# Kernel tuning notes

Measured on AMD Instinct MI355X. Metric: run time of the kernel, lower is better.

Reference implementation:

```python
import jax, jax.numpy as jnp
import numpy as np

IMG_DIM = 512
BATCH = 32


def setup_inputs() -> dict:
    key = jax.random.key(0)
    k1, k2, k3, k4, k5 = jax.random.split(key, 5)
    N, D = BATCH, IMG_DIM
    return {
        "im1": jax.random.normal(k1, (N, 3, D, D), jnp.float32),
        "im2": jax.random.normal(k2, (N, 3, D, D), jnp.float32),
        "C": jax.random.normal(k3, (N, 2, D, D), jnp.float32),
        "M1": jax.random.uniform(k4, (N, 1, D, D), jnp.float32),
        "M2": jax.random.uniform(k5, (N, 1, D, D), jnp.float32),
    }


def _grid_q(D):
    # q[0] = row coord repeated, q[1] = col coord tiled -> [2, D*D]
    x = jnp.arange(D, dtype=jnp.float32)
    return jnp.stack([jnp.repeat(x, D), jnp.tile(x, D)], axis=0)


def _get_pixel(qi, nb_x, nb_y, imflat, D):
    # qi: [N,2,HW]; nb_x, nb_y: [N,HW] integer-valued floats; imflat: [N,3,HW]
    w = (1.0 - jnp.abs(qi[:, 0] - nb_x)) * (1.0 - jnp.abs(qi[:, 1] - nb_y))  # [N,HW]
    inds = (nb_y + D * nb_x).astype(jnp.int32)  # ind = y + D*x, detached from grads
    inds = jax.lax.stop_gradient(inds)
    px = jnp.take_along_axis(imflat, inds[:, None, :], axis=2)  # [N,3,HW]
    return w[:, None, :] * px


def _masked_rp(image, mask, qi_orig, D):
    N = image.shape[0]
    HW = D * D
    imflat = image.reshape(N, 3, HW)
    qi = jnp.clip(qi_orig, 0.001, D - 1.001)  # [N,2,HW]
    fx, fy = jnp.floor(qi[:, 0]), jnp.floor(qi[:, 1])
    cx, cy = jnp.ceil(qi[:, 0]), jnp.ceil(qi[:, 1])
    res = (_get_pixel(qi, fx, fy, imflat, D)
           + _get_pixel(qi, cx, fy, imflat, D)
           + _get_pixel(qi, fx, cy, imflat, D)
           + _get_pixel(qi, cx, cy, imflat, D))  # [N,3,HW]
    oob_loss = jnp.mean((qi_orig - qi) ** 2) / (D * D) * 0.01
    res_img = res.reshape(image.shape)
    return res_img * mask, oob_loss


def _forward(im1, im2, C, M1, M2):
    N = im1.shape[0]
    D = im1.shape[2]
    q = _grid_q(D)[None]  # [1,2,HW]
    Cflat = C.reshape(N, 2, D * D)
    a, la = _masked_rp(im1, M1, q + Cflat, D)
    b, lb = _masked_rp(im2, M2, q - Cflat, D)
    return a + b, la + lb


def reference(im1, im2, C, M1, M2):
    return _forward(im1, im2, C, M1, M2)
```

## Files before the change

kernel.cpp:

```cpp
#include <hip/hip_runtime.h>


constexpr int D    = 512;
constexpr int HW   = D * D;
constexpr int NB   = 32;
constexpr int NPIX = NB * HW;
constexpr float LOSS_SCALE = (float)(0.01 / (2.0 * (double)NPIX * (double)HW));

__device__ __forceinline__ float3 sample_img(const float* __restrict__ im,
                                             float q0o, float q1o, float& oob)
{
    const float hi = (float)(512.0 - 1.001);
    float q0 = fminf(fmaxf(q0o, 0.001f), hi);
    float q1 = fminf(fmaxf(q1o, 0.001f), hi);
    float d0 = q0o - q0, d1 = q1o - q1;
    oob += d0 * d0 + d1 * d1;

    float fx = floorf(q0), fy = floorf(q1);
    float cx = ceilf(q0),  cy = ceilf(q1);
    float wfx = 1.0f - (q0 - fx), wcx = 1.0f - (cx - q0);
    float wfy = 1.0f - (q1 - fy), wcy = 1.0f - (cy - q1);

    int ix0 = (int)fx, iy0 = (int)fy, ix1 = (int)cx, iy1 = (int)cy;
    int iff = iy0 + D * ix0;
    int icf = iy0 + D * ix1;
    int ifc = iy1 + D * ix0;
    int icc = iy1 + D * ix1;

    float wff = wfx * wfy, wcf = wcx * wfy, wfc = wfx * wcy, wcc = wcx * wcy;

    float3 r;
    r.x = wff * im[iff]          + wcf * im[icf]          + wfc * im[ifc]          + wcc * im[icc];
    r.y = wff * im[HW + iff]     + wcf * im[HW + icf]     + wfc * im[HW + ifc]     + wcc * im[HW + icc];
    r.z = wff * im[2 * HW + iff] + wcf * im[2 * HW + icf] + wfc * im[2 * HW + ifc] + wcc * im[2 * HW + icc];
    return r;
}

__global__ void __launch_bounds__(256)
vm_fwd(const float* __restrict__ im1, const float* __restrict__ im2,
       const float* __restrict__ C,   const float* __restrict__ M1,
       const float* __restrict__ M2,  float* __restrict__ out)
{
    float oob = 0.0f;
    int stride = gridDim.x * blockDim.x;
    for (int idx = blockIdx.x * blockDim.x + threadIdx.x; idx < NPIX; idx += stride) {
        int n  = idx >> 18;
        int hw = idx & (HW - 1);
        float qx = (float)(hw >> 9);
        float qy = (float)(hw & (D - 1));

        const float* Cn = C + (size_t)n * 2 * HW;
        float c0 = Cn[hw];
        float c1 = Cn[HW + hw];
        float m1 = M1[idx];
        float m2 = M2[idx];

        const float* p1 = im1 + (size_t)n * 3 * HW;
        const float* p2 = im2 + (size_t)n * 3 * HW;

        float3 a = sample_img(p1, qx + c0, qy + c1, oob);
        float3 b = sample_img(p2, qx - c0, qy - c1, oob);

        size_t obase = (size_t)n * 3 * HW + hw;
        out[obase]          = a.x * m1 + b.x * m2;
        out[obase + HW]     = a.y * m1 + b.y * m2;
        out[obase + 2 * HW] = a.z * m1 + b.z * m2;
    }

    #pragma unroll
    for (int off = 32; off > 0; off >>= 1)
        oob += __shfl_down(oob, off, 64);

    __shared__ float wave_sums[4];
    int lane = threadIdx.x & 63;
    int wave = threadIdx.x >> 6;
    if (lane == 0) wave_sums[wave] = oob;
    __syncthreads();
    if (threadIdx.x == 0) {
        float s = wave_sums[0] + wave_sums[1] + wave_sums[2] + wave_sums[3];
        atomicAdd(out + (size_t)3 * NPIX, s * LOSS_SCALE);
    }
}

extern "C" void kernel_launch(void* const* d_in, const int* in_sizes, int n_in,
                              void* d_out, int out_size, void* d_ws, size_t ws_size,
                              hipStream_t stream) {
    const float* im1 = (const float*)d_in[0];
    const float* im2 = (const float*)d_in[1];
    const float* C   = (const float*)d_in[2];
    const float* M1  = (const float*)d_in[3];
    const float* M2  = (const float*)d_in[4];
    float* out = (float*)d_out;

    hipMemsetAsync(out + (size_t)3 * NPIX, 0, sizeof(float), stream);

    vm_fwd<<<8192, 256, 0, stream>>>(im1, im2, C, M1, M2, out);
}
```

Before: 417.2 us.

## Process four pixels per thread with vector loads and paired-column gathers

Each thread now handles four consecutive pixels, using float4 nontemporal loads for the flow field and masks and float4 nontemporal stores for the output. The bilinear gather fetches adjacent y neighbours as one unaligned 2-float load per row, which cuts the gather instruction count in half. The grid-stride loop is replaced by an exact launch of NPIX/1024 blocks. The trade-offs are higher register pressure and unaligned paired loads that can read one element past a row, which stays in bounds because the sample is clamped below 510.999.

```diff
diff --git a/kernel.cpp b/kernel.cpp
--- a/kernel.cpp
+++ b/kernel.cpp
@@ -7,33 +7,48 @@
 constexpr int NPIX = NB * HW;
 constexpr float LOSS_SCALE = (float)(0.01 / (2.0 * (double)NPIX * (double)HW));
 
-__device__ __forceinline__ float3 sample_img(const float* __restrict__ im,
-                                             float q0o, float q1o, float& oob)
+typedef float f4  __attribute__((ext_vector_type(4)));
+typedef float f2a4 __attribute__((ext_vector_type(2), aligned(4)));
+
+__device__ __forceinline__ f2a4 ld2(const float* p) {
+    return *(const f2a4*)p;
+}
+
+__device__ __forceinline__ void sample_add(const float* __restrict__ im,
+                                           float q0o, float q1o, float m,
+                                           float& oob, float& ax, float& ay, float& az)
 {
-    const float hi = (float)(512.0 - 1.001);
+    const float hi = 510.999f;
     float q0 = fminf(fmaxf(q0o, 0.001f), hi);
     float q1 = fminf(fmaxf(q1o, 0.001f), hi);
     float d0 = q0o - q0, d1 = q1o - q1;
     oob += d0 * d0 + d1 * d1;
 
-    float fx = floorf(q0), fy = floorf(q1);
-    float cx = ceilf(q0),  cy = ceilf(q1);
+    float fx = floorf(q0), cx = ceilf(q0);
+    float fy = floorf(q1), cy = ceilf(q1);
     float wfx = 1.0f - (q0 - fx), wcx = 1.0f - (cx - q0);
     float wfy = 1.0f - (q1 - fy), wcy = 1.0f - (cy - q1);
 
-    int ix0 = (int)fx, iy0 = (int)fy, ix1 = (int)cx, iy1 = (int)cy;
-    int iff = iy0 + D * ix0;
-    int icf = iy0 + D * ix1;
-    int ifc = iy1 + D * ix0;
-    int icc = iy1 + D * ix1;
+    int ix0 = (int)fx, ix1 = (int)cx, iy0 = (int)fy;
+    bool ysame = ((int)cy == iy0);
 
-    float wff = wfx * wfy, wcf = wcx * wfy, wfc = wfx * wcy, wcc = wcx * wcy;
+    int off0 = (ix0 << 9) + iy0;
+    int off1 = (ix1 << 9) + iy0;
 
-    float3 r;
-    r.x = wff * im[iff]          + wcf * im[icf]          + wfc * im[ifc]          + wcc * im[icc];
-    r.y = wff * im[HW + iff]     + wcf * im[HW + icf]     + wfc * im[HW + ifc]     + wcc * im[HW + icc];
-    r.z = wff * im[2 * HW + iff] + wcf * im[2 * HW + icf] + wfc * im[2 * HW + ifc] + wcc * im[2 * HW + icc];
-    return r;
+    f2a4 r0x = ld2(im + off0);
+    f2a4 r1x = ld2(im + off1);
+    f2a4 r0y = ld2(im + HW + off0);
+    f2a4 r1y = ld2(im + HW + off1);
+    f2a4 r0z = ld2(im + 2 * HW + off0);
+    f2a4 r1z = ld2(im + 2 * HW + off1);
+
+    float v0, v1;
+    v0 = ysame ? r0x.x : r0x.y;  v1 = ysame ? r1x.x : r1x.y;
+    ax += m * (wfx * (wfy * r0x.x + wcy * v0) + wcx * (wfy * r1x.x + wcy * v1));
+    v0 = ysame ? r0y.x : r0y.y;  v1 = ysame ? r1y.x : r1y.y;
+    ay += m * (wfx * (wfy * r0y.x + wcy * v0) + wcx * (wfy * r1y.x + wcy * v1));
+    v0 = ysame ? r0z.x : r0z.y;  v1 = ysame ? r1z.x : r1z.y;
+    az += m * (wfx * (wfy * r0z.x + wcy * v0) + wcx * (wfy * r1z.x + wcy * v1));
 }
 
 __global__ void __launch_bounds__(256)
@@ -41,31 +56,37 @@
        const float* __restrict__ C,   const float* __restrict__ M1,
        const float* __restrict__ M2,  float* __restrict__ out)
 {
+    int tid = blockIdx.x * 256 + threadIdx.x;
+    int pix = tid << 2;
+    int n   = pix >> 18;
+    int hw  = pix & (HW - 1);
+    float qx  = (float)(hw >> 9);
+    float qyb = (float)(hw & (D - 1));
+
+    const float* Cn = C + (size_t)n * 2 * HW;
+    f4 c0v = __builtin_nontemporal_load((const f4*)(Cn + hw));
+    f4 c1v = __builtin_nontemporal_load((const f4*)(Cn + HW + hw));
+    f4 m1v = __builtin_nontemporal_load((const f4*)(M1 + pix));
+    f4 m2v = __builtin_nontemporal_load((const f4*)(M2 + pix));
+
+    const float* p1 = im1 + (size_t)n * 3 * HW;
+    const float* p2 = im2 + (size_t)n * 3 * HW;
+
     float oob = 0.0f;
-    int stride = gridDim.x * blockDim.x;
-    for (int idx = blockIdx.x * blockDim.x + threadIdx.x; idx < NPIX; idx += stride) {
-        int n  = idx >> 18;
-        int hw = idx & (HW - 1);
-        float qx = (float)(hw >> 9);
-        float qy = (float)(hw & (D - 1));
+    f4 ox, oy, oz;
+    #pragma unroll
+    for (int j = 0; j < 4; ++j) {
+        float qy = qyb + (float)j;
+        float ax = 0.f, ay = 0.f, az = 0.f;
+        sample_add(p1, qx + c0v[j], qy + c1v[j], m1v[j], oob, ax, ay, az);
+        sample_add(p2, qx - c0v[j], qy - c1v[j], m2v[j], oob, ax, ay, az);
+        ox[j] = ax; oy[j] = ay; oz[j] = az;
+    }
 
-        const float* Cn = C + (size_t)n * 2 * HW;
-        float c0 = Cn[hw];
-        float c1 = Cn[HW + hw];
-        float m1 = M1[idx];
-        float m2 = M2[idx];
-
-        const float* p1 = im1 + (size_t)n * 3 * HW;
-        const float* p2 = im2 + (size_t)n * 3 * HW;
-
-        float3 a = sample_img(p1, qx + c0, qy + c1, oob);
-        float3 b = sample_img(p2, qx - c0, qy - c1, oob);
-
-        size_t obase = (size_t)n * 3 * HW + hw;
-        out[obase]          = a.x * m1 + b.x * m2;
-        out[obase + HW]     = a.y * m1 + b.y * m2;
-        out[obase + 2 * HW] = a.z * m1 + b.z * m2;
-    }
+    size_t obase = (size_t)n * 3 * HW + hw;
+    __builtin_nontemporal_store(ox, (f4*)(out + obase));
+    __builtin_nontemporal_store(oy, (f4*)(out + obase + HW));
+    __builtin_nontemporal_store(oz, (f4*)(out + obase + 2 * HW));
 
     #pragma unroll
     for (int off = 32; off > 0; off >>= 1)
@@ -92,7 +113,7 @@
     const float* M2  = (const float*)d_in[4];
     float* out = (float*)d_out;
 
-    hipMemsetAsync(out + (size_t)3 * NPIX, 0, sizeof(float), stream);
+    (void)hipMemsetAsync(out + (size_t)3 * NPIX, 0, sizeof(float), stream);
 
-    vm_fwd<<<8192, 256, 0, stream>>>(im1, im2, C, M1, M2, out);
+    vm_fwd<<<NPIX / 4 / 256, 256, 0, stream>>>(im1, im2, C, M1, M2, out);
 }
```

After: 444.4 us. 6.5% more time.
